# Performance work log

Hardware: AMD Instinct MI355X
Metric: run time of the kernel (lower is better)

## Reference

```python
import jax, jax.numpy as jnp
import numpy as np
import math

D_MODEL = 1024
N_HEADS = 16
HEAD_DIM = D_MODEL // N_HEADS
THETA = 10000.0


def _rope(x, cos, sin):
    # x: [b, h, s, head_dim]; cos/sin: [s, head_dim//2]
    xe = x[..., 0::2]
    xo = x[..., 1::2]
    re = xe * cos - xo * sin
    ro = xe * sin + xo * cos
    # interleave back to even/odd layout
    return jnp.stack([re, ro], axis=-1).reshape(x.shape)


def setup_inputs() -> dict:
    key = jax.random.key(0)
    k1, k2, k3, k4, k5 = jax.random.split(key, 5)
    std = math.sqrt(2.0 / (D_MODEL + D_MODEL))
    x = jax.random.normal(k1, (2, 2048, D_MODEL), dtype=jnp.float32)
    Wq = jax.random.normal(k2, (D_MODEL, D_MODEL), dtype=jnp.float32) * std
    Wk = jax.random.normal(k3, (D_MODEL, D_MODEL), dtype=jnp.float32) * std
    Wv = jax.random.normal(k4, (D_MODEL, D_MODEL), dtype=jnp.float32) * std
    Wo = jax.random.normal(k5, (D_MODEL, D_MODEL), dtype=jnp.float32) * (std / math.sqrt(2))
    return {"x": x, "Wq": Wq, "Wk": Wk, "Wv": Wv, "Wo": Wo}


def reference(x, Wq, Wk, Wv, Wo):
    b, s, d = x.shape
    h, hd = N_HEADS, HEAD_DIM
    # projections: einsum 'batch seq d_in, d_model d_in -> batch seq d_model' == x @ W.T
    def proj(W):
        y = jnp.einsum('bsd,md->bsm', x, W)
        return y.reshape(b, s, h, hd).transpose(0, 2, 1, 3)  # [b, h, s, hd]
    Q, K, V = proj(Wq), proj(Wk), proj(Wv)
    # RoPE with default positions = arange(seq)
    freqs = 1.0 / (THETA ** (jnp.arange(0, hd, 2, dtype=jnp.float32) / hd))
    angles = jnp.arange(s, dtype=jnp.float32)[:, None] * freqs[None, :]  # [s, hd//2]
    cos, sin = jnp.cos(angles), jnp.sin(angles)
    Q = _rope(Q, cos, sin)
    K = _rope(K, cos, sin)
    # naive causal attention
    scores = jnp.einsum('bhqd,bhkd->bhqk', Q, K) / math.sqrt(hd)
    causal = jnp.tril(jnp.ones((s, s), dtype=bool))
    scores = jnp.where(causal, scores, -jnp.inf)
    attn = jax.nn.softmax(scores, axis=-1)
    out = jnp.einsum('bhqk,bhkd->bhqd', attn, V)
    out = out.transpose(0, 2, 1, 3).reshape(b, s, d)
    return jnp.einsum('bsd,md->bsm', out, Wo)
```

## Files before the change

kernel.cpp:

```cpp
#include <hip/hip_runtime.h>
#include <stdint.h>
#include <stddef.h>

typedef __bf16 bf16;
typedef __bf16 bf16x8 __attribute__((ext_vector_type(8)));
typedef __bf16 bf16x4 __attribute__((ext_vector_type(4)));
typedef short short4v __attribute__((ext_vector_type(4)));
typedef float f32x4 __attribute__((ext_vector_type(4)));

#define GAS __attribute__((address_space(1)))
#define LAS __attribute__((address_space(3)))

__device__ __forceinline__ void async_load16(const void* g, void* l) {
  __builtin_amdgcn_global_load_lds((const GAS void*)g, (LAS void*)l, 16, 0, 0);
}

__device__ __forceinline__ f32x4 mfma16(bf16x4 a, bf16x4 b, f32x4 c) {
#if defined(__HIP_DEVICE_COMPILE__)
#if __has_builtin(__builtin_amdgcn_mfma_f32_16x16x16bf16_1k)
  return __builtin_amdgcn_mfma_f32_16x16x16bf16_1k(
      __builtin_bit_cast(short4v, a), __builtin_bit_cast(short4v, b), c, 0, 0, 0);
#else
  f32x4 d;
  asm volatile("v_mfma_f32_16x16x16_bf16 %0, %1, %2, %3"
               : "=v"(d)
               : "v"(a), "v"(b), "v"(c));
  return d;
#endif
#else
  (void)a; (void)b;
  return c;
#endif
}

__global__ __launch_bounds__(256) void cast_all(
    const float* __restrict__ x, const float* __restrict__ Wq,
    const float* __restrict__ Wk, const float* __restrict__ Wv,
    const float* __restrict__ Wo, bf16* __restrict__ Xh,
    bf16* __restrict__ Wqkv, bf16* __restrict__ Woh) {
  int idx = (blockIdx.x * 256 + threadIdx.x) * 4;
  const float* src;
  bf16* dst;
  float scale = 1.0f;
  if (idx < 4194304) {
    src = x + idx; dst = Xh + idx;
  } else if (idx < 7340032) {
    int j = idx - 4194304;
    if (j < 1048576) {
      src = Wq + j; scale = 0.18033688011112042f;
    } else {
      src = ((j < 2097152) ? Wk : Wv) + (j & 1048575);
    }
    dst = Wqkv + j;
  } else {
    int j = idx - 7340032;
    src = Wo + j; dst = Woh + j;
  }
  float4 v = *(const float4*)src;
  bf16x4 o;
  o[0] = (bf16)(v.x * scale); o[1] = (bf16)(v.y * scale);
  o[2] = (bf16)(v.z * scale); o[3] = (bf16)(v.w * scale);
  *(bf16x4*)dst = o;
}

__global__ __launch_bounds__(256) void gemm_qkv(
    const bf16* __restrict__ A, const bf16* __restrict__ B,
    bf16* __restrict__ Qh, bf16* __restrict__ Kh, bf16* __restrict__ Vt,
    int K) {
  __shared__ __align__(16) bf16 As[128 * 32];
  __shared__ __align__(16) bf16 Bs[128 * 32];
  const int tid = threadIdx.x;
  const int wave = tid >> 6, lane = tid & 63;
  const int bm = blockIdx.y * 128, bn = blockIdx.x * 128;
  const int wm = (wave >> 1) * 64, wn = (wave & 1) * 64;
  const int lrow = lane >> 2, lk = (lane & 3) * 8;
  const int fr = lane & 15, fk = (lane >> 4) * 8;

  f32x4 acc[4][4] = {};

  for (int kt = 0; kt < K; kt += 32) {
    __syncthreads();
#pragma unroll
    for (int c = 0; c < 2; ++c) {
      const int chunk = wave * 2 + c;
      const bf16* ga = A + (size_t)(bm + chunk * 16 + lrow) * K + kt + lk;
      async_load16(ga, (void*)(As + chunk * 512));
      const bf16* gb = B + (size_t)(bn + chunk * 16 + lrow) * K + kt + lk;
      async_load16(gb, (void*)(Bs + chunk * 512));
    }
    __syncthreads();

    bf16x8 af[4], bfr[4];
#pragma unroll
    for (int i = 0; i < 4; ++i)
      af[i] = *(const bf16x8*)&As[(wm + i * 16 + fr) * 32 + fk];
#pragma unroll
    for (int j = 0; j < 4; ++j)
      bfr[j] = *(const bf16x8*)&Bs[(wn + j * 16 + fr) * 32 + fk];
#pragma unroll
    for (int i = 0; i < 4; ++i)
#pragma unroll
      for (int j = 0; j < 4; ++j)
        acc[i][j] =
            __builtin_amdgcn_mfma_f32_16x16x32_bf16(af[i], bfr[j], acc[i][j], 0, 0, 0);
  }

  const int r0 = (lane >> 4) * 4, cc = lane & 15;
  const bool oddl = cc & 1;
#pragma unroll
  for (int i = 0; i < 4; ++i) {
    const int row0 = bm + wm + i * 16 + r0;
    const int b = row0 >> 11, s0 = row0 & 2047;
#pragma unroll
    for (int j = 0; j < 4; ++j) {
      const int col = bn + wn + j * 16 + cc;
      if (col < 2048) {
        const int hcol = col & 1023;
        const int h = hcol >> 6, d = hcol & 63;
        const int ip = d >> 1;
        const float freq = __expf((float)ip * -0.2878231366242557f);
        bf16* dst = (col < 1024 ? Qh : Kh) + ((size_t)(b * 16 + h) * 2048) * 64 + d;
#pragma unroll
        for (int r = 0; r < 4; ++r) {
          float own = acc[i][j][r];
          float oth = __shfl_xor(own, 1, 64);
          float sn, cs;
          __sincosf((float)(s0 + r) * freq, &sn, &cs);
          float res = oddl ? (oth * sn + own * cs) : (own * cs - oth * sn);
          dst[(size_t)(s0 + r) * 64] = (bf16)res;
        }
      } else {
        const int v = col - 2048, h = v >> 6, d = v & 63;
        bf16x4 o;
#pragma unroll
        for (int r = 0; r < 4; ++r) o[r] = (bf16)acc[i][j][r];
        const int s2 = (s0 & ~63) | ((s0 ^ ((d & 7) << 3)) & 63);
        *(bf16x4*)&Vt[(((size_t)b * 16 + h) * 64 + d) * 2048 + s2] = o;
      }
    }
  }
}

template <typename OutT, int BM, int BN>
__global__ __launch_bounds__(256) void gemm_bt(
    const bf16* __restrict__ A, const bf16* __restrict__ B,
    OutT* __restrict__ C, int M, int N, int K) {
  constexpr int ACH = BM / 16, NCH = (BM + BN) / 16, PW = NCH / 4;
  constexpr int FM = BM / 32, FN = BN / 32;
  __shared__ __align__(16) bf16 As[BM * 32];
  __shared__ __align__(16) bf16 Bs[BN * 32];
  const int tid = threadIdx.x;
  const int wave = tid >> 6, lane = tid & 63;
  const int bm = blockIdx.y * BM, bn = blockIdx.x * BN;
  const int wm = (wave >> 1) * (BM / 2), wn = (wave & 1) * (BN / 2);
  const int lrow = lane >> 2, lk = (lane & 3) * 8;
  const int fr = lane & 15, fk = (lane >> 4) * 8;

  f32x4 acc[FM][FN] = {};

  for (int kt = 0; kt < K; kt += 32) {
    __syncthreads();
#pragma unroll
    for (int c = 0; c < PW; ++c) {
      const int chunk = wave * PW + c;
      if (chunk < ACH) {
        const bf16* ga = A + (size_t)(bm + chunk * 16 + lrow) * K + kt + lk;
        async_load16(ga, (void*)(As + chunk * 512));
      } else {
        const int bc = chunk - ACH;
        const bf16* gb = B + (size_t)(bn + bc * 16 + lrow) * K + kt + lk;
        async_load16(gb, (void*)(Bs + bc * 512));
      }
    }
    __syncthreads();

    bf16x8 af[FM], bfr[FN];
#pragma unroll
    for (int i = 0; i < FM; ++i)
      af[i] = *(const bf16x8*)&As[(wm + i * 16 + fr) * 32 + fk];
#pragma unroll
    for (int j = 0; j < FN; ++j)
      bfr[j] = *(const bf16x8*)&Bs[(wn + j * 16 + fr) * 32 + fk];
#pragma unroll
    for (int i = 0; i < FM; ++i)
#pragma unroll
      for (int j = 0; j < FN; ++j)
        acc[i][j] =
            __builtin_amdgcn_mfma_f32_16x16x32_bf16(af[i], bfr[j], acc[i][j], 0, 0, 0);
  }

  const int r0 = (lane >> 4) * 4, cc = lane & 15;
#pragma unroll
  for (int i = 0; i < FM; ++i)
#pragma unroll
    for (int j = 0; j < FN; ++j)
#pragma unroll
      for (int r = 0; r < 4; ++r)
        C[(size_t)(bm + wm + i * 16 + r0 + r) * N + (bn + wn + j * 16 + cc)] =
            (OutT)acc[i][j][r];
}

__global__ __launch_bounds__(128, 3) void attn(const bf16* __restrict__ Qh,
                                               const bf16* __restrict__ Kh,
                                               const bf16* __restrict__ Vt,
                                               bf16* __restrict__ Oh) {
  __shared__ __align__(16) float smem[4096];
  bf16* __restrict__ Vs = (bf16*)smem;
  float* __restrict__ scratch = smem;
  const int f = blockIdx.x;
  const int j = 63 - (f >> 5);
  const int bh = f & 31;
  const int tid = threadIdx.x, w = tid >> 6, lane = tid & 63;
  const int nlo = lane & 15, g = lane >> 4;
  const int q0 = j * 32;
  const bf16* __restrict__ Qp = Qh + (size_t)bh * 131072;
  const bf16* __restrict__ Kp = Kh + (size_t)bh * 131072;
  const bf16* __restrict__ Vp = Vt + (size_t)bh * 131072;
  const int n = (j >> 1) + 1;
  const int hf = (n + 1) >> 1;
  const int t0 = w ? hf : 0;
  const int cnt = w ? (n - hf) : hf;

  bf16x8 aq[2][2];
#pragma unroll
  for (int qb = 0; qb < 2; ++qb)
#pragma unroll
    for (int ks = 0; ks < 2; ++ks)
      aq[qb][ks] =
          *(const bf16x8*)&Qp[(size_t)(q0 + qb * 16 + nlo) * 64 + ks * 32 + g * 8];

  f32x4 oacc[2][4] = {};
  float lsum[2] = {0.f, 0.f};

  const int srow = lane >> 3, soff = (lane & 7) * 8;
  const int sw = (nlo & 7) << 3;
  bf16* __restrict__ Vw = Vs + w * 4096;

  for (int it = 0; it < cnt; ++it) {
    const int i = t0 + it, kbase = i * 64;

    const bf16* vsrc = Vp + (size_t)srow * 2048 + kbase + soff;
#pragma unroll
    for (int c = 0; c < 8; ++c)
      async_load16(vsrc + (size_t)c * 16384, (void*)(Vw + c * 512));

    bf16x8 pk[4][2];
#pragma unroll
    for (int ni = 0; ni < 4; ++ni)
#pragma unroll
      for (int ks = 0; ks < 2; ++ks)
        pk[ni][ks] = *(const bf16x8*)&Kp[(size_t)(kbase + ni * 16 + nlo) * 64 +
                                         ks * 32 + g * 8];

    const bool dg = (i == n - 1);
    bf16x4 p[2][4];
#pragma unroll
    for (int qb = 0; qb < 2; ++qb) {
      f32x4 st[4] = {};
#pragma unroll
      for (int ks = 0; ks < 2; ++ks)
#pragma unroll
        for (int ni = 0; ni < 4; ++ni)
          st[ni] = __builtin_amdgcn_mfma_f32_16x16x32_bf16(pk[ni][ks], aq[qb][ks],
                                                           st[ni], 0, 0, 0);
      const int qg = q0 + qb * 16 + nlo;
      if (!dg) {
#pragma unroll
        for (int ni = 0; ni < 4; ++ni)
#pragma unroll
          for (int r = 0; r < 4; ++r) {
            float e = __builtin_amdgcn_exp2f(st[ni][r]);
            lsum[qb] += e;
            p[qb][ni][r] = (bf16)e;
          }
      } else {
#pragma unroll
        for (int ni = 0; ni < 4; ++ni) {
          const int kg0 = kbase + ni * 16 + g * 4;
#pragma unroll
          for (int r = 0; r < 4; ++r) {
            float e = __builtin_amdgcn_exp2f(st[ni][r]);
            e = (kg0 + r <= qg) ? e : 0.0f;
            lsum[qb] += e;
            p[qb][ni][r] = (bf16)e;
          }
        }
      }
    }

    asm volatile("s_waitcnt vmcnt(0)" ::: "memory");

#pragma unroll
    for (int ni = 0; ni < 4; ++ni)
#pragma unroll
      for (int mi = 0; mi < 4; ++mi) {
        bf16x4 av = *(const bf16x4*)&Vw[(mi * 16 + nlo) * 64 +
                                        ((ni * 16 + g * 4) ^ sw)];
#pragma unroll
        for (int qb = 0; qb < 2; ++qb)
          oacc[qb][mi] = mfma16(av, p[qb][ni], oacc[qb][mi]);
      }
  }

#pragma unroll
  for (int qb = 0; qb < 2; ++qb) {
    lsum[qb] += __shfl_xor(lsum[qb], 16, 64);
    lsum[qb] += __shfl_xor(lsum[qb], 32, 64);
  }

  __syncthreads();
  if (w == 1) {
#pragma unroll
    for (int qb = 0; qb < 2; ++qb) {
#pragma unroll
      for (int mi = 0; mi < 4; ++mi)
#pragma unroll
        for (int r = 0; r < 4; ++r)
          scratch[(qb * 16 + mi * 4 + r) * 64 + lane] = oacc[qb][mi][r];
      scratch[(32 + qb) * 64 + lane] = lsum[qb];
    }
  }
  __syncthreads();
  if (w == 0) {
    const int b = bh >> 4, hd = bh & 15;
#pragma unroll
    for (int qb = 0; qb < 2; ++qb) {
      const float l = lsum[qb] + scratch[(32 + qb) * 64 + lane];
      const float inv = 1.0f / l;
      const int q = q0 + qb * 16 + nlo;
#pragma unroll
      for (int mi = 0; mi < 4; ++mi) {
        bf16x4 o;
#pragma unroll
        for (int r = 0; r < 4; ++r)
          o[r] = (bf16)((oacc[qb][mi][r] +
                         scratch[(qb * 16 + mi * 4 + r) * 64 + lane]) * inv);
        *(bf16x4*)&Oh[((size_t)b * 2048 + q) * 1024 + hd * 64 + mi * 16 + g * 4] = o;
      }
    }
  }
}

extern "C" void kernel_launch(void* const* d_in, const int* in_sizes, int n_in,
                              void* d_out, int out_size, void* d_ws, size_t ws_size,
                              hipStream_t stream) {
  (void)in_sizes; (void)n_in; (void)out_size; (void)ws_size;
  const float* x = (const float*)d_in[0];
  const float* Wq = (const float*)d_in[1];
  const float* Wk = (const float*)d_in[2];
  const float* Wv = (const float*)d_in[3];
  const float* Wo = (const float*)d_in[4];
  float* out = (float*)d_out;
  char* ws = (char*)d_ws;

  bf16* Xh   = (bf16*)(ws);
  bf16* Wqkv = (bf16*)(ws + 8388608);
  bf16* Woh  = (bf16*)(ws + 14680064);
  bf16* Qh   = (bf16*)(ws + 16777216);
  bf16* Kh   = (bf16*)(ws + 25165824);
  bf16* Vt   = (bf16*)(ws + 33554432);
  bf16* Oh   = (bf16*)(ws + 41943040);

  cast_all<<<8192, 256, 0, stream>>>(x, Wq, Wk, Wv, Wo, Xh, Wqkv, Woh);
  gemm_qkv<<<dim3(24, 32), 256, 0, stream>>>(Xh, Wqkv, Qh, Kh, Vt, 1024);
  attn<<<2048, 128, 0, stream>>>(Qh, Kh, Vt, Oh);
  gemm_bt<float, 128, 128><<<dim3(8, 32), 256, 0, stream>>>(Oh, Woh, out, 4096, 1024, 1024);
}
```

Baseline: 193.8 us.

## Share K/V tiles across four waves via double-buffered LDS in attention

The attention kernel now runs 256-thread blocks covering 128 queries (four waves of 32 queries each) instead of 2 waves splitting the key range of 32 queries. K and V tiles are staged once per block into double-buffered LDS with async loads and shared by all waves, which removes the redundant global K reads and the cross-wave reduction through scratch. K is written pre-swizzled by the QKV GEMM so LDS reads avoid bank conflicts. In exchange, the grid shrinks to 512 blocks, waves idle at causal boundaries, and a barrier is added every iteration.

Result: no change. 194.8 us (+0.5%).

```diff
diff --git a/kernel.cpp b/kernel.cpp
--- a/kernel.cpp
+++ b/kernel.cpp
@@ -119,7 +119,8 @@
         const int h = hcol >> 6, d = hcol & 63;
         const int ip = d >> 1;
         const float freq = __expf((float)ip * -0.2878231366242557f);
-        bf16* dst = (col < 1024 ? Qh : Kh) + ((size_t)(b * 16 + h) * 2048) * 64 + d;
+        const bool isK = col >= 1024;
+        bf16* dst = (isK ? Kh : Qh) + ((size_t)(b * 16 + h) * 2048) * 64;
 #pragma unroll
         for (int r = 0; r < 4; ++r) {
           float own = acc[i][j][r];
@@ -127,7 +128,8 @@
           float sn, cs;
           __sincosf((float)(s0 + r) * freq, &sn, &cs);
           float res = oddl ? (oth * sn + own * cs) : (own * cs - oth * sn);
-          dst[(size_t)(s0 + r) * 64] = (bf16)res;
+          const int dd = isK ? (d ^ (((s0 + r) & 7) << 3)) : d;
+          dst[(size_t)(s0 + r) * 64 + dd] = (bf16)res;
         }
       } else {
         const int v = col - 2048, h = v >> 6, d = v & 63;
@@ -200,26 +202,22 @@
             (OutT)acc[i][j][r];
 }
 
-__global__ __launch_bounds__(128, 3) void attn(const bf16* __restrict__ Qh,
+__global__ __launch_bounds__(256, 2) void attn(const bf16* __restrict__ Qh,
                                                const bf16* __restrict__ Kh,
                                                const bf16* __restrict__ Vt,
                                                bf16* __restrict__ Oh) {
-  __shared__ __align__(16) float smem[4096];
-  bf16* __restrict__ Vs = (bf16*)smem;
-  float* __restrict__ scratch = smem;
+  __shared__ __align__(16) bf16 Ks[2][64 * 64];
+  __shared__ __align__(16) bf16 Vs[2][64 * 64];
   const int f = blockIdx.x;
-  const int j = 63 - (f >> 5);
+  const int j = 15 - (f >> 5);
   const int bh = f & 31;
   const int tid = threadIdx.x, w = tid >> 6, lane = tid & 63;
   const int nlo = lane & 15, g = lane >> 4;
-  const int q0 = j * 32;
+  const int q0 = j * 128, qw0 = q0 + w * 32;
   const bf16* __restrict__ Qp = Qh + (size_t)bh * 131072;
   const bf16* __restrict__ Kp = Kh + (size_t)bh * 131072;
   const bf16* __restrict__ Vp = Vt + (size_t)bh * 131072;
-  const int n = (j >> 1) + 1;
-  const int hf = (n + 1) >> 1;
-  const int t0 = w ? hf : 0;
-  const int cnt = w ? (n - hf) : hf;
+  const int n = 2 * (j + 1);
 
   bf16x8 aq[2][2];
 #pragma unroll
@@ -227,79 +225,98 @@
 #pragma unroll
     for (int ks = 0; ks < 2; ++ks)
       aq[qb][ks] =
-          *(const bf16x8*)&Qp[(size_t)(q0 + qb * 16 + nlo) * 64 + ks * 32 + g * 8];
+          *(const bf16x8*)&Qp[(size_t)(qw0 + qb * 16 + nlo) * 64 + ks * 32 + g * 8];
 
   f32x4 oacc[2][4] = {};
   float lsum[2] = {0.f, 0.f};
-
-  const int srow = lane >> 3, soff = (lane & 7) * 8;
   const int sw = (nlo & 7) << 3;
-  bf16* __restrict__ Vw = Vs + w * 4096;
-
-  for (int it = 0; it < cnt; ++it) {
-    const int i = t0 + it, kbase = i * 64;
-
-    const bf16* vsrc = Vp + (size_t)srow * 2048 + kbase + soff;
-#pragma unroll
-    for (int c = 0; c < 8; ++c)
-      async_load16(vsrc + (size_t)c * 16384, (void*)(Vw + c * 512));
-
-    bf16x8 pk[4][2];
-#pragma unroll
-    for (int ni = 0; ni < 4; ++ni)
-#pragma unroll
-      for (int ks = 0; ks < 2; ++ks)
-        pk[ni][ks] = *(const bf16x8*)&Kp[(size_t)(kbase + ni * 16 + nlo) * 64 +
-                                         ks * 32 + g * 8];
-
-    const bool dg = (i == n - 1);
-    bf16x4 p[2][4];
-#pragma unroll
-    for (int qb = 0; qb < 2; ++qb) {
-      f32x4 st[4] = {};
-#pragma unroll
-      for (int ks = 0; ks < 2; ++ks)
-#pragma unroll
-        for (int ni = 0; ni < 4; ++ni)
-          st[ni] = __builtin_amdgcn_mfma_f32_16x16x32_bf16(pk[ni][ks], aq[qb][ks],
-                                                           st[ni], 0, 0, 0);
-      const int qg = q0 + qb * 16 + nlo;
-      if (!dg) {
-#pragma unroll
-        for (int ni = 0; ni < 4; ++ni)
-#pragma unroll
-          for (int r = 0; r < 4; ++r) {
-            float e = __builtin_amdgcn_exp2f(st[ni][r]);
-            lsum[qb] += e;
-            p[qb][ni][r] = (bf16)e;
-          }
-      } else {
-#pragma unroll
-        for (int ni = 0; ni < 4; ++ni) {
-          const int kg0 = kbase + ni * 16 + g * 4;
-#pragma unroll
-          for (int r = 0; r < 4; ++r) {
-            float e = __builtin_amdgcn_exp2f(st[ni][r]);
-            e = (kg0 + r <= qg) ? e : 0.0f;
-            lsum[qb] += e;
-            p[qb][ni][r] = (bf16)e;
+
+  const int srow = w * 16 + (lane >> 3);
+  const int soff = (lane & 7) * 8;
+
+  auto stage = [&](int buf, int kbase) {
+    async_load16(Kp + (size_t)(kbase + srow) * 64 + soff,
+                 (void*)(Ks[buf] + w * 1024));
+    async_load16(Kp + (size_t)(kbase + srow + 8) * 64 + soff,
+                 (void*)(Ks[buf] + w * 1024 + 512));
+    async_load16(Vp + (size_t)srow * 2048 + kbase + soff,
+                 (void*)(Vs[buf] + w * 1024));
+    async_load16(Vp + (size_t)(srow + 8) * 2048 + kbase + soff,
+                 (void*)(Vs[buf] + w * 1024 + 512));
+  };
+
+  stage(0, 0);
+  __syncthreads();
+
+  for (int i = 0; i < n; ++i) {
+    const int buf = i & 1, kbase = i * 64;
+    if (i + 1 < n) stage(buf ^ 1, (i + 1) * 64);
+
+    if (kbase <= qw0 + 31) {
+      const bf16* __restrict__ Kw = Ks[buf];
+      const bf16* __restrict__ Vw = Vs[buf];
+
+      bf16x8 pk[4][2];
+#pragma unroll
+      for (int ni = 0; ni < 4; ++ni)
+#pragma unroll
+        for (int ks = 0; ks < 2; ++ks)
+          pk[ni][ks] = *(const bf16x8*)&Kw[(ni * 16 + nlo) * 64 +
+                                           ((ks * 32 + g * 8) ^ sw)];
+
+      const bool dg = (kbase + 63 > qw0);
+      bf16x4 p[2][4];
+#pragma unroll
+      for (int qb = 0; qb < 2; ++qb) {
+        f32x4 st[4] = {};
+#pragma unroll
+        for (int ks = 0; ks < 2; ++ks)
+#pragma unroll
+          for (int ni = 0; ni < 4; ++ni)
+            st[ni] = __builtin_amdgcn_mfma_f32_16x16x32_bf16(pk[ni][ks], aq[qb][ks],
+                                                             st[ni], 0, 0, 0);
+        const int qg = qw0 + qb * 16 + nlo;
+        if (!dg) {
+#pragma unroll
+          for (int ni = 0; ni < 4; ++ni)
+#pragma unroll
+            for (int r = 0; r < 4; ++r) {
+              float e = __builtin_amdgcn_exp2f(st[ni][r]);
+              lsum[qb] += e;
+              p[qb][ni][r] = (bf16)e;
+            }
+        } else {
+#pragma unroll
+          for (int ni = 0; ni < 4; ++ni) {
+            const int kg0 = kbase + ni * 16 + g * 4;
+#pragma unroll
+            for (int r = 0; r < 4; ++r) {
+              float e = __builtin_amdgcn_exp2f(st[ni][r]);
+              e = (kg0 + r <= qg) ? e : 0.0f;
+              lsum[qb] += e;
+              p[qb][ni][r] = (bf16)e;
+            }
           }
         }
       }
-    }
-
-    asm volatile("s_waitcnt vmcnt(0)" ::: "memory");
-
-#pragma unroll
-    for (int ni = 0; ni < 4; ++ni)
-#pragma unroll
-      for (int mi = 0; mi < 4; ++mi) {
-        bf16x4 av = *(const bf16x4*)&Vw[(mi * 16 + nlo) * 64 +
-                                        ((ni * 16 + g * 4) ^ sw)];
-#pragma unroll
-        for (int qb = 0; qb < 2; ++qb)
-          oacc[qb][mi] = mfma16(av, p[qb][ni], oacc[qb][mi]);
-      }
+
+      bf16x4 av[4][4];
+#pragma unroll
+      for (int ni = 0; ni < 4; ++ni)
+#pragma unroll
+        for (int mi = 0; mi < 4; ++mi)
+          av[ni][mi] = *(const bf16x4*)&Vw[(mi * 16 + nlo) * 64 +
+                                           ((ni * 16 + g * 4) ^ sw)];
+#pragma unroll
+      for (int ni = 0; ni < 4; ++ni)
+#pragma unroll
+        for (int mi = 0; mi < 4; ++mi)
+#pragma unroll
+          for (int qb = 0; qb < 2; ++qb)
+            oacc[qb][mi] = mfma16(av[ni][mi], p[qb][ni], oacc[qb][mi]);
+    }
+
+    __syncthreads();
   }
 
 #pragma unroll
@@ -308,35 +325,17 @@
     lsum[qb] += __shfl_xor(lsum[qb], 32, 64);
   }
 
-  __syncthreads();
-  if (w == 1) {
-#pragma unroll
-    for (int qb = 0; qb < 2; ++qb) {
-#pragma unroll
-      for (int mi = 0; mi < 4; ++mi)
-#pragma unroll
-        for (int r = 0; r < 4; ++r)
-          scratch[(qb * 16 + mi * 4 + r) * 64 + lane] = oacc[qb][mi][r];
-      scratch[(32 + qb) * 64 + lane] = lsum[qb];
-    }
-  }
-  __syncthreads();
-  if (w == 0) {
-    const int b = bh >> 4, hd = bh & 15;
-#pragma unroll
-    for (int qb = 0; qb < 2; ++qb) {
-      const float l = lsum[qb] + scratch[(32 + qb) * 64 + lane];
-      const float inv = 1.0f / l;
-      const int q = q0 + qb * 16 + nlo;
-#pragma unroll
-      for (int mi = 0; mi < 4; ++mi) {
-        bf16x4 o;
-#pragma unroll
-        for (int r = 0; r < 4; ++r)
-          o[r] = (bf16)((oacc[qb][mi][r] +
-                         scratch[(qb * 16 + mi * 4 + r) * 64 + lane]) * inv);
-        *(bf16x4*)&Oh[((size_t)b * 2048 + q) * 1024 + hd * 64 + mi * 16 + g * 4] = o;
-      }
+  const int bb = bh >> 4, hd = bh & 15;
+#pragma unroll
+  for (int qb = 0; qb < 2; ++qb) {
+    const float inv = 1.0f / lsum[qb];
+    const int q = qw0 + qb * 16 + nlo;
+#pragma unroll
+    for (int mi = 0; mi < 4; ++mi) {
+      bf16x4 o;
+#pragma unroll
+      for (int r = 0; r < 4; ++r) o[r] = (bf16)(oacc[qb][mi][r] * inv);
+      *(bf16x4*)&Oh[((size_t)bb * 2048 + q) * 1024 + hd * 64 + mi * 16 + g * 4] = o;
     }
   }
 }
@@ -363,6 +362,6 @@
 
   cast_all<<<8192, 256, 0, stream>>>(x, Wq, Wk, Wv, Wo, Xh, Wqkv, Woh);
   gemm_qkv<<<dim3(24, 32), 256, 0, stream>>>(Xh, Wqkv, Qh, Kh, Vt, 1024);
-  attn<<<2048, 128, 0, stream>>>(Qh, Kh, Vt, Oh);
+  attn<<<512, 256, 0, stream>>>(Qh, Kh, Vt, Oh);
   gemm_bt<float, 128, 128><<<dim3(8, 32), 256, 0, stream>>>(Oh, Woh, out, 4096, 1024, 1024);
 }
```
